# Performance work log

Hardware: AMD Instinct MI355X
Metric: run time of the kernel (lower is better)

## Reference

```python
import jax, jax.numpy as jnp
import numpy as np

N_NODES = 100000
N_EDGES = 1000000
D = 128          # input_dim == hidden_dim (required: h = zeros_like(nh) accumulates src_nf)
OUT = 128
NUM_TYPES = 5


def setup_inputs() -> dict:
    key = jax.random.key(0)
    ks = jax.random.split(key, 7)
    nh = jax.random.normal(ks[0], (N_NODES, D), dtype=jnp.float32)
    edge_y = jax.random.randint(ks[1], (N_EDGES,), 0, NUM_TYPES, dtype=jnp.int64)
    edge_index = jax.random.randint(ks[2], (2, N_EDGES), 0, N_NODES, dtype=jnp.int64)
    # nn.Linear weights, scaled for numerical sanity
    W_nf = jax.random.normal(ks[3], (D, D), dtype=jnp.float32) * 0.08
    W_attn = jax.random.normal(ks[4], (1, 2 * D), dtype=jnp.float32) * 0.08
    W_out = jax.random.normal(ks[5], (OUT, 2 * D), dtype=jnp.float32) * 0.08
    b_out = jax.random.normal(ks[6], (OUT,), dtype=jnp.float32) * 0.01
    return {"nh": nh, "edge_y": edge_y, "edge_index": edge_index,
            "W_nf": W_nf, "W_attn": W_attn, "W_out": W_out, "b_out": b_out}


def reference(nh, edge_y, edge_index, W_nf, W_attn, W_out, b_out):
    n = nh.shape[0]
    src, dst = edge_index[0], edge_index[1]

    # nf_lin applied once per node, then gathered per edge (same math as
    # self.nf_lin(nh[src]) since Linear is per-row)
    nfl = nh @ W_nf.T                                  # [N, D]
    src_nf = nfl[src]                                  # [E, D]
    dst_nf = nfl[dst]                                  # [E, D]

    # attn(cat([src_nf, dst_nf])) == src_nf @ a_src + dst_nf @ a_dst
    a_src, a_dst = W_attn[0, :D], W_attn[0, D:]
    ef = src_nf @ a_src + dst_nf @ a_dst               # [E]
    ef = jnp.where(ef >= 0, ef, 0.2 * ef)              # LeakyReLU(0.2)

    # scatter_softmax per (edge_type, dst) group: the per-type loop with
    # scatter_softmax over dst is exactly a segment softmax over composite
    # segments seg = dst*5 + type; the summed per-type scatter_adds equal
    # one segment_sum over dst.
    seg = dst * NUM_TYPES + edge_y                     # [E]
    num_seg = n * NUM_TYPES
    m = jax.ops.segment_max(ef, seg, num_segments=num_seg)
    ex = jnp.exp(ef - m[seg])
    denom = jax.ops.segment_sum(ex, seg, num_segments=num_seg)
    alpha = ex / denom[seg]                            # [E]

    h = jax.ops.segment_sum(alpha[:, None] * src_nf, dst, num_segments=n)  # [N, D]

    nf = jnp.concatenate([nh, h], axis=-1) @ W_out.T + b_out
    return jax.nn.relu(nf)
```

## Files before the change

kernel.cpp:

```cpp
#include <hip/hip_runtime.h>

#define NTYPES 5
#define EPB 4096
#define BKSH 7
#define BKDST 128
#define SUBD 32
#define CAP 1024

typedef _Float16 half8 __attribute__((ext_vector_type(8)));
typedef _Float16 half4v __attribute__((ext_vector_type(4)));
typedef float float4v __attribute__((ext_vector_type(4)));

__device__ __forceinline__ void stage_f32(
    _Float16* lds, const float* __restrict__ g, int rows, int stride4, int off4,
    int grow0, int nmax, int t)
{
  const float4* g4 = (const float4*)g;
  for (int i = t; i < rows * 32; i += 256) {
    int row = i >> 5, q = i & 31;
    float4 v = make_float4(0.f, 0.f, 0.f, 0.f);
    int gr = grow0 + row;
    if (gr < nmax) v = g4[(size_t)gr * stride4 + off4 + q];
    half4v hv = { (_Float16)v.x, (_Float16)v.y, (_Float16)v.z, (_Float16)v.w };
    int byte = row * 256 + ((q * 8) ^ ((row & 7) << 4));
    *(half4v*)((char*)lds + byte) = hv;
  }
}

__device__ __forceinline__ half8 frag_ld(const _Float16* lds, int row, int khw) {
  int byte = row * 256 + ((khw * 2) ^ ((row & 7) << 4));
  return *(const half8*)((const char*)lds + byte);
}

__device__ __forceinline__ half8 cvt8(float4 v0, float4 v1) {
  half8 a;
  a[0] = (_Float16)v0.x; a[1] = (_Float16)v0.y; a[2] = (_Float16)v0.z; a[3] = (_Float16)v0.w;
  a[4] = (_Float16)v1.x; a[5] = (_Float16)v1.y; a[6] = (_Float16)v1.z; a[7] = (_Float16)v1.w;
  return a;
}

__global__ __launch_bounds__(256) void k_gemm0(
    const float* __restrict__ nh, const float* __restrict__ Wnf,
    const float* __restrict__ Wattn,
    float* __restrict__ s_src, float* __restrict__ s_dst,
    _Float16* __restrict__ nfl, _Float16* __restrict__ nh16, int n)
{
  __shared__ _Float16 wh[128 * 128];
  const int t = threadIdx.x, lane = t & 63, wv = t >> 6;
  const int r16 = lane & 15, g = lane >> 4;
  stage_f32(wh, Wnf, 128, 32, 0, 0, 1 << 30, t);
  __syncthreads();
  const int nchunk = (n + 63) >> 6;
  for (int c = blockIdx.x; c < nchunk; c += gridDim.x) {
    const int base = c << 6;
    const int arow = base + wv * 16 + r16;
    const bool ok = arow < n;
    const float4* nh4 = (const float4*)(nh + (size_t)arow * 128);
    const float4 z = make_float4(0.f, 0.f, 0.f, 0.f);
    float4 av[8];
    #pragma unroll
    for (int s = 0; s < 4; ++s) {
      av[2 * s]     = ok ? nh4[s * 8 + g * 2]     : z;
      av[2 * s + 1] = ok ? nh4[s * 8 + g * 2 + 1] : z;
    }
    float4v acc[8];
    #pragma unroll
    for (int nf = 0; nf < 8; ++nf) acc[nf] = (float4v){0.f, 0.f, 0.f, 0.f};
    #pragma unroll
    for (int s = 0; s < 4; ++s) {
      half8 a = cvt8(av[2 * s], av[2 * s + 1]);
      if (ok) *(half8*)(nh16 + (size_t)arow * 128 + s * 32 + g * 8) = a;
      #pragma unroll
      for (int nf = 0; nf < 8; ++nf)
        acc[nf] = __builtin_amdgcn_mfma_f32_16x16x32_f16(
            frag_ld(wh, nf * 16 + r16, s * 32 + g * 8), a, acc[nf], 0, 0, 0);
    }
    if (ok) {
      size_t ro = (size_t)arow * 128;
      #pragma unroll
      for (int nf = 0; nf < 8; ++nf) {
        half4v hv = { (_Float16)acc[nf][0], (_Float16)acc[nf][1],
                      (_Float16)acc[nf][2], (_Float16)acc[nf][3] };
        *(half4v*)(nfl + ro + nf * 16 + g * 4) = hv;
      }
    }
    float ss = 0.f, sd = 0.f;
    #pragma unroll
    for (int nf = 0; nf < 8; ++nf) {
      float4 wa = *(const float4*)(Wattn + nf * 16 + g * 4);
      float4 wd = *(const float4*)(Wattn + 128 + nf * 16 + g * 4);
      ss += acc[nf][0]*wa.x + acc[nf][1]*wa.y + acc[nf][2]*wa.z + acc[nf][3]*wa.w;
      sd += acc[nf][0]*wd.x + acc[nf][1]*wd.y + acc[nf][2]*wd.z + acc[nf][3]*wd.w;
    }
    ss += __shfl_xor(ss, 16); ss += __shfl_xor(ss, 32);
    sd += __shfl_xor(sd, 16); sd += __shfl_xor(sd, 32);
    if (ok && g == 0) { s_src[arow] = ss; s_dst[arow] = sd; }
  }
}

__global__ __launch_bounds__(256) void k_hist(
    const int* __restrict__ dsts, int* __restrict__ cnt, int e, int nbk, int nblk)
{
  __shared__ int hist[1024];
  const int t = threadIdx.x, b = blockIdx.x;
  for (int k = t; k < nbk; k += 256) hist[k] = 0;
  __syncthreads();
  const int i0 = b * EPB;
  const int iend = min(i0 + EPB, e);
  for (int i = i0 + t; i < iend; i += 256)
    atomicAdd(&hist[dsts[i] >> BKSH], 1);
  __syncthreads();
  for (int k = t; k < nbk; k += 256) cnt[k * nblk + b] = hist[k];
}

__global__ __launch_bounds__(256) void k_scan1(
    const int* __restrict__ deg, int* __restrict__ base, int* __restrict__ bsum, int n)
{
  __shared__ int ws[4];
  int t = threadIdx.x;
  int g0 = blockIdx.x * 1024 + t * 4;
  int4 v = make_int4(0, 0, 0, 0);
  if (g0 + 3 < n) v = *(const int4*)(deg + g0);
  else {
    if (g0     < n) v.x = deg[g0];
    if (g0 + 1 < n) v.y = deg[g0 + 1];
    if (g0 + 2 < n) v.z = deg[g0 + 2];
    if (g0 + 3 < n) v.w = deg[g0 + 3];
  }
  int s = v.x + v.y + v.z + v.w;
  int inc = s;
  #pragma unroll
  for (int d = 1; d < 64; d <<= 1) {
    int o = __shfl_up(inc, d);
    if ((t & 63) >= d) inc += o;
  }
  int wid = t >> 6;
  if ((t & 63) == 63) ws[wid] = inc;
  __syncthreads();
  int woff = 0;
  for (int w = 0; w < wid; ++w) woff += ws[w];
  int exc = woff + inc - s;
  if (g0 + 3 < n) {
    *(int4*)(base + g0) = make_int4(exc, exc + v.x, exc + v.x + v.y, exc + v.x + v.y + v.z);
  } else {
    if (g0     < n) base[g0]     = exc;
    if (g0 + 1 < n) base[g0 + 1] = exc + v.x;
    if (g0 + 2 < n) base[g0 + 2] = exc + v.x + v.y;
  }
  if (t == 255) bsum[blockIdx.x] = woff + inc;
}

__global__ __launch_bounds__(256) void k_scan2(
    const int* __restrict__ bsum, int* __restrict__ boff, int nb)
{
  __shared__ int ws[4];
  int t = threadIdx.x;
  int x = t < nb ? bsum[t] : 0;
  int inc = x;
  #pragma unroll
  for (int d = 1; d < 64; d <<= 1) {
    int o = __shfl_up(inc, d);
    if ((t & 63) >= d) inc += o;
  }
  int wid = t >> 6;
  if ((t & 63) == 63) ws[wid] = inc;
  __syncthreads();
  int woff = 0;
  for (int w = 0; w < wid; ++w) woff += ws[w];
  if (t < nb) boff[t] = woff + inc - x;
}

__global__ __launch_bounds__(256) void k_scan3(
    int* __restrict__ base, const int* __restrict__ boff, int n)
{
  int i = blockIdx.x * 256 + threadIdx.x;
  if (i < n) base[i] += boff[i >> 10];
}

__global__ __launch_bounds__(256) void k_scatter2(
    const int* __restrict__ ei, const int* __restrict__ ey,
    const int* __restrict__ cnt_s, unsigned* __restrict__ rec,
    int e, int nbk, int nblk)
{
  __shared__ int cur[1024];
  const int t = threadIdx.x, b = blockIdx.x;
  for (int k = t; k < nbk; k += 256) cur[k] = cnt_s[k * nblk + b];
  __syncthreads();
  const int i0 = b * EPB;
  const int iend = min(i0 + EPB, e);
  for (int i = i0 + t; i < iend; i += 256) {
    int s = ei[i], d = ei[e + i], ty = ey[i];
    int pos = atomicAdd(&cur[d >> BKSH], 1);
    rec[pos] = (unsigned)s | ((unsigned)ty << 17) | ((unsigned)(d & (BKDST - 1)) << 20);
  }
}

__global__ __launch_bounds__(256) void k_agg2(
    const unsigned* __restrict__ rec, const int* __restrict__ cnt_s,
    const float* __restrict__ s_src, const float* __restrict__ s_dst,
    const _Float16* __restrict__ nfl, _Float16* __restrict__ h,
    int n, int e, int nbk, int nblk)
{
  __shared__ unsigned ord[CAP];
  __shared__ float efl[CAP];
  __shared__ int dcnt[SUBD];
  __shared__ int dbase[SUBD + 1];
  __shared__ float sdl[SUBD];
  const int t = threadIdx.x;
  const int sb = blockIdx.x;
  const int d0 = sb << 5;
  const int ndst = min(SUBD, n - d0);
  const int k = sb >> 2;
  const int sub = sb & 3;
  const int bs = cnt_s[k * nblk];
  const int be = (k + 1 < nbk) ? cnt_s[(k + 1) * nblk] : e;
  const int cnt = be - bs;
  if (t < SUBD) {
    dcnt[t] = 0;
    if (t < ndst) sdl[t] = s_dst[d0 + t];
  }
  __syncthreads();
  const int g = t >> 4, l = t & 15;

  for (int i = t; i < cnt; i += 256) {
    int dl = (rec[bs + i] >> 20) & 127;
    if ((dl >> 5) == sub) atomicAdd(&dcnt[dl & 31], 1);
  }
  __syncthreads();
  if (t < SUBD) {
    int v = dcnt[t];
    int inc = v;
    #pragma unroll
    for (int dd = 1; dd < SUBD; dd <<= 1) {
      int o = __shfl_up(inc, dd);
      if (t >= dd) inc += o;
    }
    dbase[t] = inc - v;
    dcnt[t]  = inc - v;
    if (t == SUBD - 1) dbase[SUBD] = inc;
  }
  __syncthreads();
  const int total = dbase[SUBD];

  if (total <= CAP) {
    for (int i = t; i < cnt; i += 256) {
      unsigned p = rec[bs + i];
      int dl = (p >> 20) & 127;
      if ((dl >> 5) == sub) {
        int pos = atomicAdd(&dcnt[dl & 31], 1);
        ord[pos] = p;
      }
    }
    __syncthreads();
    for (int i = t; i < total; i += 256) {
      unsigned p = ord[i];
      float ef = s_src[p & 0x1FFFF] + sdl[(p >> 20) & 31];
      efl[i] = ef >= 0.f ? ef : 0.2f * ef;
    }
    __syncthreads();
    for (int di = g; di < ndst; di += 16) {
      int s0 = dbase[di], deg = dbase[di + 1] - s0;
      float acc[8] = {0.f, 0.f, 0.f, 0.f, 0.f, 0.f, 0.f, 0.f};
      if (deg > 0) {
        float mx[NTYPES];
        #pragma unroll
        for (int tt = 0; tt < NTYPES; ++tt) mx[tt] = -1e30f;
        for (int j0 = 0; j0 < deg; j0 += 16) {
          int jj = j0 + l;
          bool ok = jj < deg;
          float ef = ok ? efl[s0 + jj] : -1e30f;
          int ty = ok ? (int)((ord[s0 + jj] >> 17) & 7) : 7;
          #pragma unroll
          for (int tt = 0; tt < NTYPES; ++tt) {
            float v = (ty == tt) ? ef : -1e30f;
            v = fmaxf(v, __shfl_xor(v, 1)); v = fmaxf(v, __shfl_xor(v, 2));
            v = fmaxf(v, __shfl_xor(v, 4)); v = fmaxf(v, __shfl_xor(v, 8));
            mx[tt] = fmaxf(mx[tt], v);
          }
        }
        float sm[NTYPES];
        #pragma unroll
        for (int tt = 0; tt < NTYPES; ++tt) sm[tt] = 0.f;
        for (int j0 = 0; j0 < deg; j0 += 16) {
          int jj = j0 + l;
          bool ok = jj < deg;
          int ty = ok ? (int)((ord[s0 + jj] >> 17) & 7) : 7;
          float ex = ok ? __expf(efl[s0 + jj] - mx[ty]) : 0.f;
          if (ok) efl[s0 + jj] = ex;
          #pragma unroll
          for (int tt = 0; tt < NTYPES; ++tt) {
            float v = (ty == tt) ? ex : 0.f;
            v += __shfl_xor(v, 1); v += __shfl_xor(v, 2);
            v += __shfl_xor(v, 4); v += __shfl_xor(v, 8);
            sm[tt] += v;
          }
        }
        float rsm[NTYPES];
        #pragma unroll
        for (int tt = 0; tt < NTYPES; ++tt) rsm[tt] = sm[tt] > 0.f ? 1.f / sm[tt] : 0.f;
        int j = 0;
        for (; j + 4 <= deg; j += 4) {
          unsigned p0 = ord[s0 + j],     p1 = ord[s0 + j + 1];
          unsigned p2 = ord[s0 + j + 2], p3 = ord[s0 + j + 3];
          float a0 = efl[s0 + j]     * rsm[(p0 >> 17) & 7];
          float a1 = efl[s0 + j + 1] * rsm[(p1 >> 17) & 7];
          float a2 = efl[s0 + j + 2] * rsm[(p2 >> 17) & 7];
          float a3 = efl[s0 + j + 3] * rsm[(p3 >> 17) & 7];
          half8 x0 = *(const half8*)(nfl + (size_t)(p0 & 0x1FFFF) * 128 + l * 8);
          half8 x1 = *(const half8*)(nfl + (size_t)(p1 & 0x1FFFF) * 128 + l * 8);
          half8 x2 = *(const half8*)(nfl + (size_t)(p2 & 0x1FFFF) * 128 + l * 8);
          half8 x3 = *(const half8*)(nfl + (size_t)(p3 & 0x1FFFF) * 128 + l * 8);
          #pragma unroll
          for (int kk = 0; kk < 8; ++kk) acc[kk] = fmaf(a0, (float)x0[kk], acc[kk]);
          #pragma unroll
          for (int kk = 0; kk < 8; ++kk) acc[kk] = fmaf(a1, (float)x1[kk], acc[kk]);
          #pragma unroll
          for (int kk = 0; kk < 8; ++kk) acc[kk] = fmaf(a2, (float)x2[kk], acc[kk]);
          #pragma unroll
          for (int kk = 0; kk < 8; ++kk) acc[kk] = fmaf(a3, (float)x3[kk], acc[kk]);
        }
        for (; j < deg; ++j) {
          unsigned p0 = ord[s0 + j];
          float a0 = efl[s0 + j] * rsm[(p0 >> 17) & 7];
          half8 x0 = *(const half8*)(nfl + (size_t)(p0 & 0x1FFFF) * 128 + l * 8);
          #pragma unroll
          for (int kk = 0; kk < 8; ++kk) acc[kk] = fmaf(a0, (float)x0[kk], acc[kk]);
        }
      }
      half8 hv;
      #pragma unroll
      for (int kk = 0; kk < 8; ++kk) hv[kk] = (_Float16)acc[kk];
      *(half8*)(h + (size_t)(d0 + di) * 128 + l * 8) = hv;
    }
  } else {
    const int gb = (t & 63) & 48;
    for (int di = g; di < ndst; di += 16) {
      const int want = sub * SUBD + di;
      float mx[NTYPES], sm[NTYPES];
      #pragma unroll
      for (int tt = 0; tt < NTYPES; ++tt) { mx[tt] = -1e30f; sm[tt] = 0.f; }
      for (int j0 = 0; j0 < cnt; j0 += 16) {
        int jj = j0 + l;
        unsigned p = (jj < cnt) ? rec[bs + jj] : 0xFFFFFFFFu;
        bool mine = (p != 0xFFFFFFFFu) && (int)((p >> 20) & 127) == want;
        float ef = -1e30f; int ty = 7;
        if (mine) {
          ef = s_src[p & 0x1FFFF] + sdl[di];
          ef = ef >= 0.f ? ef : 0.2f * ef;
          ty = (p >> 17) & 7;
        }
        #pragma unroll
        for (int tt = 0; tt < NTYPES; ++tt) {
          float v = (mine && ty == tt) ? ef : -1e30f;
          v = fmaxf(v, __shfl_xor(v, 1)); v = fmaxf(v, __shfl_xor(v, 2));
          v = fmaxf(v, __shfl_xor(v, 4)); v = fmaxf(v, __shfl_xor(v, 8));
          mx[tt] = fmaxf(mx[tt], v);
        }
      }
      for (int j0 = 0; j0 < cnt; j0 += 16) {
        int jj = j0 + l;
        unsigned p = (jj < cnt) ? rec[bs + jj] : 0xFFFFFFFFu;
        bool mine = (p != 0xFFFFFFFFu) && (int)((p >> 20) & 127) == want;
        float ex = 0.f; int ty = 7;
        if (mine) {
          float ef = s_src[p & 0x1FFFF] + sdl[di];
          ef = ef >= 0.f ? ef : 0.2f * ef;
          ty = (p >> 17) & 7;
          ex = __expf(ef - mx[ty]);
        }
        #pragma unroll
        for (int tt = 0; tt < NTYPES; ++tt) {
          float v = (ty == tt) ? ex : 0.f;
          v += __shfl_xor(v, 1); v += __shfl_xor(v, 2);
          v += __shfl_xor(v, 4); v += __shfl_xor(v, 8);
          sm[tt] += v;
        }
      }
      float rsm[NTYPES];
      #pragma unroll
      for (int tt = 0; tt < NTYPES; ++tt) rsm[tt] = sm[tt] > 0.f ? 1.f / sm[tt] : 0.f;
      float acc[8] = {0.f, 0.f, 0.f, 0.f, 0.f, 0.f, 0.f, 0.f};
      for (int j0 = 0; j0 < cnt; j0 += 16) {
        int jj = j0 + l;
        unsigned p = (jj < cnt) ? rec[bs + jj] : 0xFFFFFFFFu;
        bool mine = (p != 0xFFFFFFFFu) && (int)((p >> 20) & 127) == want;
        float al = 0.f;
        if (mine) {
          float ef = s_src[p & 0x1FFFF] + sdl[di];
          ef = ef >= 0.f ? ef : 0.2f * ef;
          int ty = (p >> 17) & 7;
          al = __expf(ef - mx[ty]) * rsm[ty];
        }
        unsigned pv = mine ? p : 0xFFFFFFFFu;
        for (int jj2 = 0; jj2 < 16; ++jj2) {
          unsigned pp = __shfl(pv, gb + jj2);
          float aa = __shfl(al, gb + jj2);
          if (pp != 0xFFFFFFFFu) {
            half8 x = *(const half8*)(nfl + (size_t)(pp & 0x1FFFF) * 128 + l * 8);
            #pragma unroll
            for (int kk = 0; kk < 8; ++kk) acc[kk] = fmaf(aa, (float)x[kk], acc[kk]);
          }
        }
      }
      half8 hv;
      #pragma unroll
      for (int kk = 0; kk < 8; ++kk) hv[kk] = (_Float16)acc[kk];
      *(half8*)(h + (size_t)(d0 + di) * 128 + l * 8) = hv;
    }
  }
}

__global__ __launch_bounds__(256) void k_gemmO(
    const _Float16* __restrict__ nh16, const _Float16* __restrict__ hbuf,
    const float* __restrict__ Wout, const float* __restrict__ bias,
    float* __restrict__ out, int n)
{
  __shared__ _Float16 w1[64 * 128], w2[64 * 128];
  const int t = threadIdx.x, lane = t & 63, wv = t >> 6;
  const int r16 = lane & 15, g = lane >> 4;
  const int jhalf = blockIdx.x & 1;
  stage_f32(w1, Wout, 64, 64, 0,  jhalf * 64, 1 << 30, t);
  stage_f32(w2, Wout, 64, 64, 32, jhalf * 64, 1 << 30, t);
  float4 bv4[4];
  #pragma unroll
  for (int nf = 0; nf < 4; ++nf)
    bv4[nf] = *(const float4*)(bias + jhalf * 64 + nf * 16 + g * 4);
  __syncthreads();
  const int nchunk = (n + 63) >> 6;
  const int gstride = gridDim.x >> 1;
  int c = blockIdx.x >> 1;
  half8 c1[4], c2[4];
  if (c < nchunk) {
    int arow = (c << 6) + wv * 16 + r16;
    bool ok = arow < n;
    #pragma unroll
    for (int s = 0; s < 4; ++s) {
      c1[s] = ok ? *(const half8*)(nh16 + (size_t)arow * 128 + s * 32 + g * 8) : (half8){};
      c2[s] = ok ? *(const half8*)(hbuf + (size_t)arow * 128 + s * 32 + g * 8) : (half8){};
    }
  }
  for (; c < nchunk; c += gstride) {
    const int base = c << 6;
    const int arow = base + wv * 16 + r16;
    int cn = c + gstride;
    half8 n1[4] = {}, n2[4] = {};
    if (cn < nchunk) {
      int nrow = (cn << 6) + wv * 16 + r16;
      bool ok = nrow < n;
      #pragma unroll
      for (int s = 0; s < 4; ++s) {
        n1[s] = ok ? *(const half8*)(nh16 + (size_t)nrow * 128 + s * 32 + g * 8) : (half8){};
        n2[s] = ok ? *(const half8*)(hbuf + (size_t)nrow * 128 + s * 32 + g * 8) : (half8){};
      }
    }
    float4v acc[4];
    #pragma unroll
    for (int nf = 0; nf < 4; ++nf) acc[nf] = (float4v){0.f, 0.f, 0.f, 0.f};
    #pragma unroll
    for (int s = 0; s < 4; ++s) {
      #pragma unroll
      for (int nf = 0; nf < 4; ++nf) {
        acc[nf] = __builtin_amdgcn_mfma_f32_16x16x32_f16(
            frag_ld(w1, nf * 16 + r16, s * 32 + g * 8), c1[s], acc[nf], 0, 0, 0);
        acc[nf] = __builtin_amdgcn_mfma_f32_16x16x32_f16(
            frag_ld(w2, nf * 16 + r16, s * 32 + g * 8), c2[s], acc[nf], 0, 0, 0);
      }
    }
    if (arow < n) {
      size_t ro = (size_t)arow * 128 + jhalf * 64;
      #pragma unroll
      for (int nf = 0; nf < 4; ++nf) {
        float4 o;
        o.x = fmaxf(acc[nf][0] + bv4[nf].x, 0.f);
        o.y = fmaxf(acc[nf][1] + bv4[nf].y, 0.f);
        o.z = fmaxf(acc[nf][2] + bv4[nf].z, 0.f);
        o.w = fmaxf(acc[nf][3] + bv4[nf].w, 0.f);
        *(float4*)(out + ro + nf * 16 + g * 4) = o;
      }
    }
    #pragma unroll
    for (int s = 0; s < 4; ++s) { c1[s] = n1[s]; c2[s] = n2[s]; }
  }
}

extern "C" void kernel_launch(void* const* d_in, const int* in_sizes, int n_in,
                              void* d_out, int out_size, void* d_ws, size_t ws_size,
                              hipStream_t stream) {
  const float* nh     = (const float*)d_in[0];
  const int*   edge_y = (const int*)d_in[1];
  const int*   ei     = (const int*)d_in[2];
  const float* W_nf   = (const float*)d_in[3];
  const float* W_attn = (const float*)d_in[4];
  const float* W_out  = (const float*)d_in[5];
  const float* b_out  = (const float*)d_in[6];
  float* out = (float*)d_out;
  const int n = in_sizes[0] / 128;
  const int e = in_sizes[1];
  const int nbk  = (n + BKDST - 1) >> BKSH;
  const int nblk = (e + EPB - 1) / EPB;
  const int ncnt = nbk * nblk;
  const int nb2  = (ncnt + 1023) / 1024;
  const int nsb  = (n + SUBD - 1) / SUBD;

  _Float16* nfl_h = (_Float16*)d_ws;
  _Float16* nh16  = nfl_h + (size_t)n * 128;
  _Float16* h_h   = nh16 + (size_t)n * 128;
  float* s_src = (float*)(h_h + (size_t)n * 128);
  float* s_dst = s_src + n;
  int*   cnt   = (int*)(s_dst + n);
  int*   bsum  = cnt + ncnt;
  int*   boff  = bsum + 256;
  unsigned* rec = (unsigned*)(boff + 256);

  k_gemm0<<<1280, 256, 0, stream>>>(nh, W_nf, W_attn, s_src, s_dst, nfl_h, nh16, n);
  k_hist<<<nblk, 256, 0, stream>>>(ei + e, cnt, e, nbk, nblk);
  k_scan1<<<nb2, 256, 0, stream>>>(cnt, cnt, bsum, ncnt);
  k_scan2<<<1, 256, 0, stream>>>(bsum, boff, nb2);
  k_scan3<<<(ncnt + 255) / 256, 256, 0, stream>>>(cnt, boff, ncnt);
  k_scatter2<<<nblk, 256, 0, stream>>>(ei, edge_y, cnt, rec, e, nbk, nblk);
  k_agg2<<<nsb, 256, 0, stream>>>(rec, cnt, s_src, s_dst, nfl_h, h_h, n, e, nbk, nblk);
  k_gemmO<<<1280, 256, 0, stream>>>(nh16, h_h, W_out, b_out, out, n);
}
```

Baseline: 179.3 us.

## Split first GEMM output columns across block pairs and move attention scores to separate kernel

The node-feature GEMM kernel now has each pair of blocks share a row chunk, with each block computing half of the output columns. This halves LDS weight staging and the accumulator registers, which should allow more resident blocks. The attention score dot products move to a new lightweight kernel that rereads the fp16 nfl rows, since a half-width block can no longer compute them alone. In exchange, every nh row is loaded twice from global memory, there is an extra kernel launch, and the scores are now computed from fp16-rounded features.

```diff
diff --git a/kernel.cpp b/kernel.cpp
--- a/kernel.cpp
+++ b/kernel.cpp
@@ -41,19 +41,18 @@
 
 __global__ __launch_bounds__(256) void k_gemm0(
     const float* __restrict__ nh, const float* __restrict__ Wnf,
-    const float* __restrict__ Wattn,
-    float* __restrict__ s_src, float* __restrict__ s_dst,
     _Float16* __restrict__ nfl, _Float16* __restrict__ nh16, int n)
 {
-  __shared__ _Float16 wh[128 * 128];
+  __shared__ _Float16 wh[64 * 128];
   const int t = threadIdx.x, lane = t & 63, wv = t >> 6;
   const int r16 = lane & 15, g = lane >> 4;
-  stage_f32(wh, Wnf, 128, 32, 0, 0, 1 << 30, t);
+  const int jhalf = blockIdx.x & 1;
+  stage_f32(wh, Wnf, 64, 32, 0, jhalf * 64, 128, t);
   __syncthreads();
   const int nchunk = (n + 63) >> 6;
-  for (int c = blockIdx.x; c < nchunk; c += gridDim.x) {
-    const int base = c << 6;
-    const int arow = base + wv * 16 + r16;
+  const int cstride = gridDim.x >> 1;
+  for (int c = blockIdx.x >> 1; c < nchunk; c += cstride) {
+    const int arow = (c << 6) + wv * 16 + r16;
     const bool ok = arow < n;
     const float4* nh4 = (const float4*)(nh + (size_t)arow * 128);
     const float4 z = make_float4(0.f, 0.f, 0.f, 0.f);
@@ -63,39 +62,53 @@
       av[2 * s]     = ok ? nh4[s * 8 + g * 2]     : z;
       av[2 * s + 1] = ok ? nh4[s * 8 + g * 2 + 1] : z;
     }
-    float4v acc[8];
-    #pragma unroll
-    for (int nf = 0; nf < 8; ++nf) acc[nf] = (float4v){0.f, 0.f, 0.f, 0.f};
+    float4v acc[4];
+    #pragma unroll
+    for (int nf = 0; nf < 4; ++nf) acc[nf] = (float4v){0.f, 0.f, 0.f, 0.f};
     #pragma unroll
     for (int s = 0; s < 4; ++s) {
       half8 a = cvt8(av[2 * s], av[2 * s + 1]);
-      if (ok) *(half8*)(nh16 + (size_t)arow * 128 + s * 32 + g * 8) = a;
-      #pragma unroll
-      for (int nf = 0; nf < 8; ++nf)
+      if (ok && (s >> 1) == jhalf)
+        *(half8*)(nh16 + (size_t)arow * 128 + s * 32 + g * 8) = a;
+      #pragma unroll
+      for (int nf = 0; nf < 4; ++nf)
         acc[nf] = __builtin_amdgcn_mfma_f32_16x16x32_f16(
             frag_ld(wh, nf * 16 + r16, s * 32 + g * 8), a, acc[nf], 0, 0, 0);
     }
     if (ok) {
-      size_t ro = (size_t)arow * 128;
-      #pragma unroll
-      for (int nf = 0; nf < 8; ++nf) {
+      size_t ro = (size_t)arow * 128 + jhalf * 64;
+      #pragma unroll
+      for (int nf = 0; nf < 4; ++nf) {
         half4v hv = { (_Float16)acc[nf][0], (_Float16)acc[nf][1],
                       (_Float16)acc[nf][2], (_Float16)acc[nf][3] };
         *(half4v*)(nfl + ro + nf * 16 + g * 4) = hv;
       }
     }
-    float ss = 0.f, sd = 0.f;
-    #pragma unroll
-    for (int nf = 0; nf < 8; ++nf) {
-      float4 wa = *(const float4*)(Wattn + nf * 16 + g * 4);
-      float4 wd = *(const float4*)(Wattn + 128 + nf * 16 + g * 4);
-      ss += acc[nf][0]*wa.x + acc[nf][1]*wa.y + acc[nf][2]*wa.z + acc[nf][3]*wa.w;
-      sd += acc[nf][0]*wd.x + acc[nf][1]*wd.y + acc[nf][2]*wd.z + acc[nf][3]*wd.w;
-    }
-    ss += __shfl_xor(ss, 16); ss += __shfl_xor(ss, 32);
-    sd += __shfl_xor(sd, 16); sd += __shfl_xor(sd, 32);
-    if (ok && g == 0) { s_src[arow] = ss; s_dst[arow] = sd; }
-  }
+  }
+}
+
+__global__ __launch_bounds__(256) void k_attn(
+    const _Float16* __restrict__ nfl, const float* __restrict__ Wattn,
+    float* __restrict__ s_src, float* __restrict__ s_dst, int n)
+{
+  const int grp = threadIdx.x >> 4, l = threadIdx.x & 15;
+  const int node = blockIdx.x * 16 + grp;
+  float4 wa0 = *(const float4*)(Wattn + l * 8);
+  float4 wa1 = *(const float4*)(Wattn + l * 8 + 4);
+  float4 wd0 = *(const float4*)(Wattn + 128 + l * 8);
+  float4 wd1 = *(const float4*)(Wattn + 128 + l * 8 + 4);
+  if (node >= n) return;
+  half8 x = *(const half8*)(nfl + (size_t)node * 128 + l * 8);
+  float ss = (float)x[0]*wa0.x + (float)x[1]*wa0.y + (float)x[2]*wa0.z + (float)x[3]*wa0.w
+           + (float)x[4]*wa1.x + (float)x[5]*wa1.y + (float)x[6]*wa1.z + (float)x[7]*wa1.w;
+  float sd = (float)x[0]*wd0.x + (float)x[1]*wd0.y + (float)x[2]*wd0.z + (float)x[3]*wd0.w
+           + (float)x[4]*wd1.x + (float)x[5]*wd1.y + (float)x[6]*wd1.z + (float)x[7]*wd1.w;
+  #pragma unroll
+  for (int m = 1; m <= 8; m <<= 1) {
+    ss += __shfl_xor(ss, m);
+    sd += __shfl_xor(sd, m);
+  }
+  if (l == 0) { s_src[node] = ss; s_dst[node] = sd; }
 }
 
 __global__ __launch_bounds__(256) void k_hist(
@@ -440,8 +453,7 @@
     }
   }
   for (; c < nchunk; c += gstride) {
-    const int base = c << 6;
-    const int arow = base + wv * 16 + r16;
+    const int arow = (c << 6) + wv * 16 + r16;
     int cn = c + gstride;
     half8 n1[4] = {}, n2[4] = {};
     if (cn < nchunk) {
@@ -512,7 +524,8 @@
   int*   boff  = bsum + 256;
   unsigned* rec = (unsigned*)(boff + 256);
 
-  k_gemm0<<<1280, 256, 0, stream>>>(nh, W_nf, W_attn, s_src, s_dst, nfl_h, nh16, n);
+  k_gemm0<<<1280, 256, 0, stream>>>(nh, W_nf, nfl_h, nh16, n);
+  k_attn<<<(n + 15) / 16, 256, 0, stream>>>(nfl_h, W_attn, s_src, s_dst, n);
   k_hist<<<nblk, 256, 0, stream>>>(ei + e, cnt, e, nbk, nblk);
   k_scan1<<<nb2, 256, 0, stream>>>(cnt, cnt, bsum, ncnt);
   k_scan2<<<1, 256, 0, stream>>>(bsum, boff, nb2);
```

Result: slower. 187.9 us (+4.8%).
